# Kernel optimization log

Hardware: AMD Instinct MI355X
Metric: run time of the kernel (lower is better)

## Reference

```python
import jax, jax.numpy as jnp
import numpy as np

B, S, DIM = 2, 2048, 2048
QH, KVH = 32, 8
HD = DIM // QH            # 64
KV_DIM = HD * KVH         # 512
MAX_LEN = 2048
SCALE = HD ** -0.5
NEG_INF = -1e30


def _rope_cache(seq_len, head_dim, max_len, theta=10000.0, factor=8.0):
    # faithful to generate_sin_cos_pos_emb (causal branch, offset=0),
    # cache built at max_len then sliced to seq_len by the caller
    idx = np.arange(0, head_dim, 2, dtype=np.float64) / head_dim
    inv_freq = 1.0 / theta ** idx
    if factor > 1.0:
        seq_eff = max(max_len, max_len)  # generate called with seq_len=max_length
        adj = (factor * seq_eff / max_len - (factor - 1.0)) ** (head_dim / (head_dim - 2.0))
        inv_freq = 1.0 / (theta * adj) ** idx
    pos = np.arange(0, max_len, dtype=np.float64)
    freqs = np.einsum('i,j->ij', pos, inv_freq)
    emb = np.concatenate([freqs, freqs], axis=-1)  # [max_len, head_dim]
    cos = jnp.asarray(np.cos(emb)[:seq_len], dtype=jnp.float32)
    sin = jnp.asarray(np.sin(emb)[:seq_len], dtype=jnp.float32)
    return cos, sin


def _rotate_half(x):
    x1, x2 = jnp.split(x, 2, axis=-1)
    return jnp.concatenate([-x2, x1], axis=-1)


def _apply_rope(x, cos, sin):
    # x: [B, H, S, D]; cos/sin: [S, D]
    return x * cos + _rotate_half(x) * sin


def setup_inputs() -> dict:
    key = jax.random.key(0)
    ks = jax.random.split(key, 11)
    s = 0.02
    return {
        'query': jax.random.normal(ks[0], (B, S, DIM), jnp.float32),
        'key':   jax.random.normal(ks[1], (B, S, DIM), jnp.float32),
        'value': jax.random.normal(ks[2], (B, S, DIM), jnp.float32),
        'w_q': jax.random.normal(ks[3], (DIM, DIM), jnp.float32) * s,
        'b_q': jnp.zeros((DIM,), jnp.float32),
        'w_k': jax.random.normal(ks[4], (DIM, KV_DIM), jnp.float32) * s,
        'b_k': jnp.zeros((KV_DIM,), jnp.float32),
        'w_v': jax.random.normal(ks[5], (DIM, KV_DIM), jnp.float32) * s,
        'b_v': jnp.zeros((KV_DIM,), jnp.float32),
        'w_o': jax.random.normal(ks[6], (DIM, DIM), jnp.float32) * s,
        'b_o': jnp.zeros((DIM,), jnp.float32),
    }


def reference(query, key, value, w_q, b_q, w_k, b_k, w_v, b_v, w_o, b_o):
    # projections (weights stored as [in, out])
    q = query @ w_q + b_q                                    # [B,S,DIM]
    k = key   @ w_k + b_k                                    # [B,S,KV_DIM]
    v = value @ w_v + b_v                                    # [B,S,KV_DIM]

    q = q.reshape(B, S, QH, HD).transpose(0, 2, 1, 3)        # [B,QH,S,HD]
    k = k.reshape(B, S, KVH, HD).transpose(0, 2, 1, 3)       # [B,KVH,S,HD]
    v = v.reshape(B, S, KVH, HD).transpose(0, 2, 1, 3)       # [B,KVH,S,HD]

    cos, sin = _rope_cache(S, HD, MAX_LEN)
    q = _apply_rope(q, cos, sin)
    k = _apply_rope(k, cos, sin)

    # GQA: group queries per kv head (equivalent to repeat_interleave on K/V)
    G = QH // KVH
    qg = q.reshape(B, KVH, G, S, HD)
    scores = jnp.einsum('bhgqd,bhkd->bhgqk', qg, k) * SCALE  # [B,KVH,G,S,S]
    causal = jnp.tril(jnp.ones((S, S), dtype=bool))
    scores = jnp.where(causal, scores, NEG_INF)
    probs = jax.nn.softmax(scores, axis=-1)
    ctx = jnp.einsum('bhgqk,bhkd->bhgqd', probs, v)          # [B,KVH,G,S,HD]
    ctx = ctx.reshape(B, QH, S, HD).transpose(0, 2, 1, 3).reshape(B, S, DIM)
    return ctx @ w_o + b_o                                   # [B,S,DIM]
```

## Files before the change

kernel.cpp:

```cpp
#include <hip/hip_runtime.h>
#include <hip/hip_bf16.h>

typedef __hip_bfloat16 bf16_t;
typedef __attribute__((ext_vector_type(8))) short bf16x8;
typedef __attribute__((ext_vector_type(4))) float f32x4;

#define S_LEN   2048
#define D_MODEL 2048
#define N_QH    32
#define N_KVH   8
#define HEAD_D  64
#define KV_D    512
#define M_ROWS  4096
#define QK_SCALE (0.125f * 1.44269504088896340736f)
#define NQT     16

__global__ void rope_table_kernel(float* __restrict__ cosT, float* __restrict__ sinT) {
    int pos = blockIdx.x * 2 + (threadIdx.x >> 5);
    int j   = threadIdx.x & 31;
    double invf = pow(10000.0, -(double)(2 * j) / 64.0);
    double a = (double)pos * invf;
    cosT[pos * 32 + j] = (float)cos(a);
    sinT[pos * 32 + j] = (float)sin(a);
}

__global__ void wt_conv_all_kernel(const float* __restrict__ wq, const float* __restrict__ wk,
                                   const float* __restrict__ wv, const float* __restrict__ wo,
                                   bf16_t* __restrict__ tq, bf16_t* __restrict__ tk,
                                   bf16_t* __restrict__ tv, bf16_t* __restrict__ to) {
    __shared__ float tile[32][33];
    const int x = blockIdx.x;
    const float* W; bf16_t* Wt; int N, nb;
    if (x < 64)       { W = wq; Wt = tq; N = D_MODEL; nb = x; }
    else if (x < 80)  { W = wk; Wt = tk; N = KV_D;    nb = x - 64; }
    else if (x < 96)  { W = wv; Wt = tv; N = KV_D;    nb = x - 80; }
    else              { W = wo; Wt = to; N = D_MODEL; nb = x - 96; }
    const int K = D_MODEL;
    int n0 = nb * 32, k0 = blockIdx.y * 32;
    int tx = threadIdx.x & 31, ty = threadIdx.x >> 5;
#pragma unroll
    for (int i = 0; i < 4; i++) {
        int r = ty + i * 8;
        tile[r][tx] = W[(size_t)(k0 + r) * N + n0 + tx];
    }
    __syncthreads();
#pragma unroll
    for (int i = 0; i < 4; i++) {
        int r = ty + i * 8;
        Wt[(size_t)(n0 + r) * K + k0 + tx] = __float2bfloat16(tile[tx][r]);
    }
}

struct __align__(8) bf16x4s { bf16_t x, y, z, w; };

__device__ __forceinline__ void async_copy16(const bf16_t* g, bf16_t* l) {
    __builtin_amdgcn_global_load_lds((const __attribute__((address_space(1))) void*)g,
                                     (__attribute__((address_space(3))) void*)l, 16, 0, 0);
}

template <int ROPE, int OUTF32, int QSCALE>
__global__ __launch_bounds__(256, 2)
void gqa_gemm_kernel(const bf16_t* __restrict__ A, const bf16_t* __restrict__ Bt,
                     const float* __restrict__ bias, void* __restrict__ Cout,
                     int M, int N, int K,
                     const float* __restrict__ cosT, const float* __restrict__ sinT) {
    __shared__ __align__(16) bf16_t As[128 * 64];
    __shared__ __align__(16) bf16_t Bs[128 * 64];

    const int t = threadIdx.x;
    const int bx = blockIdx.x;
    const int xcd = bx & 7, j = bx >> 3;
    const int am0 = (((xcd >> 1) << 3) + (j >> 3)) * 128;
    const int bn0 = (((xcd & 1) << 3) + (j & 7)) * 128;

    const int l = t & 63, w = t >> 6;
    const int wr = w >> 1, wc = w & 1;
    const int lr = l & 15, lk = l >> 4;

    f32x4 acc[4][4];
#pragma unroll
    for (int i = 0; i < 4; i++)
#pragma unroll
        for (int jx = 0; jx < 4; jx++) acc[i][jx] = (f32x4)0.0f;

    const int r0 = t >> 3;
    const int c  = (t & 7) ^ (r0 & 7);
    const bf16_t* aptr = A + (size_t)(am0 + r0) * K + c * 8;
    const bf16_t* bptr = Bt + (size_t)(bn0 + r0) * K + c * 8;
    bf16_t* aLds = As + r0 * 64 + (t & 7) * 8;
    bf16_t* bLds = Bs + r0 * 64 + (t & 7) * 8;

    for (int k0 = 0; k0 < K; k0 += 64) {
#pragma unroll
        for (int s = 0; s < 4; ++s) {
            async_copy16(aptr + (size_t)(s * 32) * K + k0, aLds + s * 2048);
            async_copy16(bptr + (size_t)(s * 32) * K + k0, bLds + s * 2048);
        }
        __syncthreads();

        bf16x8 af[4][2], bfr[4][2];
#pragma unroll
        for (int mi = 0; mi < 4; mi++)
#pragma unroll
            for (int ks = 0; ks < 2; ks++)
                af[mi][ks] = *(const bf16x8*)&As[(wr * 64 + mi * 16 + lr) * 64 +
                                 ((ks * 32 + lk * 8) ^ ((lr & 7) << 3))];
#pragma unroll
        for (int ni = 0; ni < 4; ni++)
#pragma unroll
            for (int ks = 0; ks < 2; ks++)
                bfr[ni][ks] = *(const bf16x8*)&Bs[(wc * 64 + ni * 16 + lr) * 64 +
                                  ((ks * 32 + lk * 8) ^ ((lr & 7) << 3))];
#pragma unroll
        for (int mi = 0; mi < 4; mi++)
#pragma unroll
            for (int ni = 0; ni < 4; ni++)
#pragma unroll
                for (int ks = 0; ks < 2; ks++)
                    acc[mi][ni] = __builtin_amdgcn_mfma_f32_16x16x32_bf16(
                        af[mi][ks], bfr[ni][ks], acc[mi][ni], 0, 0, 0);
        __syncthreads();
    }

#pragma unroll
    for (int mi = 0; mi < 4; mi++) {
#pragma unroll
        for (int reg = 0; reg < 4; reg++) {
            int row = am0 + wr * 64 + mi * 16 + lk * 4 + reg;
            if (OUTF32) {
                float* out = (float*)Cout;
#pragma unroll
                for (int ni = 0; ni < 4; ni++) {
                    int col = bn0 + wc * 64 + ni * 16 + lr;
                    out[(size_t)row * N + col] = acc[mi][ni][reg] + bias[col];
                }
            } else if (ROPE) {
                bf16_t* out = (bf16_t*)Cout;
                int pos = row & (S_LEN - 1);
#pragma unroll
                for (int np = 0; np < 2; np++) {
                    int jj = np * 16 + lr;
                    float cs = cosT[pos * 32 + jj];
                    float sn = sinT[pos * 32 + jj];
                    int col1 = bn0 + wc * 64 + np * 16 + lr;
                    float x1 = acc[mi][np][reg] + bias[col1];
                    float x2 = acc[mi][np + 2][reg] + bias[col1 + 32];
                    float o1 = x1 * cs - x2 * sn;
                    float o2 = x2 * cs + x1 * sn;
                    if (QSCALE) { o1 *= QK_SCALE; o2 *= QK_SCALE; }
                    out[(size_t)row * N + col1]      = __float2bfloat16(o1);
                    out[(size_t)row * N + col1 + 32] = __float2bfloat16(o2);
                }
            } else {
                bf16_t* out = (bf16_t*)Cout;
#pragma unroll
                for (int ni = 0; ni < 4; ni++) {
                    int col = bn0 + wc * 64 + ni * 16 + lr;
                    out[(size_t)row * N + col] =
                        __float2bfloat16(acc[mi][ni][reg] + bias[col]);
                }
            }
        }
    }
}

__global__ __launch_bounds__(256, 2)
void gqa_kvc_kernel(const float* __restrict__ Key, const float* __restrict__ Val,
                    const float* __restrict__ Query,
                    const bf16_t* __restrict__ Wtk, const bf16_t* __restrict__ Wtv,
                    const float* __restrict__ bk, const float* __restrict__ bv,
                    bf16_t* __restrict__ Kout, bf16_t* __restrict__ VtOut,
                    bf16_t* __restrict__ Qbf,
                    const float* __restrict__ cosT, const float* __restrict__ sinT) {
    __shared__ __align__(16) char smem[33792];
    bf16_t* As = (bf16_t*)smem;
    bf16_t* Bs = (bf16_t*)(smem + 8192);
    float*  VtE = (float*)smem;

    const int bx = blockIdx.x;
    const int t = threadIdx.x;

    if (bx >= 512) {
        int tid = (bx - 512) * 256 + t;
        const int total = M_ROWS * D_MODEL / 4;
#pragma unroll 4
        for (int i = tid; i < total; i += 512 * 256) {
            float4 v = ((const float4*)Query)[i];
            bf16x4s o;
            o.x = __float2bfloat16(v.x);
            o.y = __float2bfloat16(v.y);
            o.z = __float2bfloat16(v.z);
            o.w = __float2bfloat16(v.w);
            ((bf16x4s*)Qbf)[i] = o;
        }
        return;
    }

    constexpr int K = D_MODEL;
    const int xcd = bx & 7;
    const int jj  = bx >> 3;
    const int z   = xcd >> 2;
    const int am0 = (((xcd & 3) << 3) + (jj >> 3)) * 128;
    const int bn0 = (jj & 7) * 64;

    const float* A32  = z ? Val : Key;
    const bf16_t* Bt  = z ? Wtv : Wtk;
    const float* bias = z ? bv : bk;

    const int l = t & 63, w = t >> 6;
    const int lr = l & 15, lk = l >> 4;

    f32x4 acc[2][4];
#pragma unroll
    for (int i = 0; i < 2; i++)
#pragma unroll
        for (int jx = 0; jx < 4; jx++) acc[i][jx] = (f32x4)0.0f;

    const int srow = t >> 2;
    const int scol = (t & 3) * 8;
    const float*  aptr = A32 + (size_t)(am0 + srow) * K + scol;
    const bf16_t* bptr = Bt + (size_t)(bn0 + srow) * K + scol;
    bf16_t* bLds = Bs + t * 8;

    for (int k0 = 0; k0 < K; k0 += 32) {
        async_copy16(bptr + k0, bLds);
#pragma unroll
        for (int rb = 0; rb < 2; ++rb) {
            const float* ap = aptr + (size_t)(rb * 64) * K + k0;
            float4 v0 = ((const float4*)ap)[0];
            float4 v1 = ((const float4*)ap)[1];
            union { bf16x8 v; bf16_t e[8]; } u;
            u.e[0] = __float2bfloat16(v0.x); u.e[1] = __float2bfloat16(v0.y);
            u.e[2] = __float2bfloat16(v0.z); u.e[3] = __float2bfloat16(v0.w);
            u.e[4] = __float2bfloat16(v1.x); u.e[5] = __float2bfloat16(v1.y);
            u.e[6] = __float2bfloat16(v1.z); u.e[7] = __float2bfloat16(v1.w);
            *(bf16x8*)&As[rb * 2048 + t * 8] = u.v;
        }
        __syncthreads();

        bf16x8 af[2], bfr[4];
#pragma unroll
        for (int mi = 0; mi < 2; mi++)
            af[mi] = *(const bf16x8*)&As[(w * 32 + mi * 16 + lr) * 32 + lk * 8];
#pragma unroll
        for (int ni = 0; ni < 4; ni++)
            bfr[ni] = *(const bf16x8*)&Bs[(ni * 16 + lr) * 32 + lk * 8];
#pragma unroll
        for (int mi = 0; mi < 2; mi++)
#pragma unroll
            for (int ni = 0; ni < 4; ni++)
                acc[mi][ni] = __builtin_amdgcn_mfma_f32_16x16x32_bf16(af[mi], bfr[ni],
                                                                      acc[mi][ni], 0, 0, 0);
        __syncthreads();
    }

    if (z == 0) {
#pragma unroll
        for (int mi = 0; mi < 2; mi++)
#pragma unroll
            for (int reg = 0; reg < 4; reg++) {
                int row = am0 + w * 32 + mi * 16 + lk * 4 + reg;
                int pos = row & (S_LEN - 1);
#pragma unroll
                for (int np = 0; np < 2; np++) {
                    int j = np * 16 + lr;
                    float cs = cosT[pos * 32 + j];
                    float sn = sinT[pos * 32 + j];
                    int col1 = bn0 + np * 16 + lr;
                    float x1 = acc[mi][np][reg] + bias[col1];
                    float x2 = acc[mi][np + 2][reg] + bias[col1 + 32];
                    Kout[(size_t)row * KV_D + col1]      = __float2bfloat16(x1 * cs - x2 * sn);
                    Kout[(size_t)row * KV_D + col1 + 32] = __float2bfloat16(x2 * cs + x1 * sn);
                }
            }
    } else {
#pragma unroll
        for (int mi = 0; mi < 2; mi++)
#pragma unroll
            for (int reg = 0; reg < 4; reg++)
#pragma unroll
                for (int ni = 0; ni < 4; ni++)
                    VtE[(w * 64 + ni * 16 + lr) * 33 + mi * 16 + lk * 4 + reg] =
                        acc[mi][ni][reg] + bias[bn0 + ni * 16 + lr];
        __syncthreads();
        const int d = l;
        const int bI = am0 >> 11;
        const int kvhI = bn0 >> 6;
        const int sl = (am0 & (S_LEN - 1)) + w * 32;
        bf16_t* dst = VtOut + ((size_t)(bI * N_KVH + kvhI) * HEAD_D + d) * S_LEN + sl;
        const float* src = &VtE[(w * 64 + d) * 33];
#pragma unroll
        for (int cc = 0; cc < 4; cc++) {
            union { bf16x8 v; bf16_t e[8]; } u;
#pragma unroll
            for (int j = 0; j < 8; j++) u.e[j] = __float2bfloat16(src[cc * 8 + j]);
            *(bf16x8*)(dst + cc * 8) = u.v;
        }
    }
}

__device__ __forceinline__ void stage_K8(const bf16_t* KB, bf16_t* dst, int kt, int t) {
    const int skey = t >> 3;
    const int c    = (t & 7) ^ (skey & 7);
    async_copy16(KB + (size_t)(kt * 64 + skey) * KV_D + c * 8, dst + t * 8);
}
__device__ __forceinline__ void stage_V8(const bf16_t* VTb, bf16_t* dst, int kt, int t) {
    const int sd = t >> 3;
    const int c  = (t & 7) ^ (sd & 7);
    async_copy16(VTb + (size_t)sd * S_LEN + kt * 64 + c * 8, dst + t * 8);
}

__global__ __launch_bounds__(512, 4)
void gqa_attn_kernel(const bf16_t* __restrict__ Q, const bf16_t* __restrict__ Kb,
                     const bf16_t* __restrict__ VT, bf16_t* __restrict__ Ctx) {
    __shared__ __align__(16) bf16_t Ks[2][64 * 64];
    __shared__ __align__(16) bf16_t Vs[2][64 * 64];
    __shared__ __align__(16) bf16_t Pw[8][16 * 72];

    const int t = threadIdx.x, l = t & 63, w = t >> 6;
    const int lr = l & 15, lk = l >> 4;

    const int flat = blockIdx.x;
    const int xcd = flat & 7, j0 = flat >> 3;
    const int combo  = xcd * 2 + (j0 >> 5);
    const int within = j0 & 31;
    const int b   = combo >> 3;
    const int kvh = combo & 7;
    const int h   = kvh * 4 + (within >> 3);
    const int p   = within & 7;

    const bf16_t* KB  = Kb + (size_t)b * S_LEN * KV_D + kvh * HEAD_D;
    const bf16_t* VTb = VT + ((size_t)(b * N_KVH + kvh) * HEAD_D) * S_LEN;

#pragma unroll
    for (int half = 0; half < 2; ++half) {
        const int qt  = half ? (NQT - 1 - p) : p;
        const int q0w = qt * 128 + w * 16;
        const int qg  = q0w + lr;

        bf16x8 qf[2];
        {
            const bf16_t* qrow = Q + ((size_t)(b * S_LEN + qg)) * D_MODEL + h * HEAD_D;
            qf[0] = *(const bf16x8*)(qrow + lk * 8);
            qf[1] = *(const bf16x8*)(qrow + 32 + lk * 8);
        }

        float lrow = 0.f;
        f32x4 oaccT[4];
#pragma unroll
        for (int df = 0; df < 4; df++) oaccT[df] = (f32x4)0.0f;

        const int nkt = 2 * qt + 2;

        stage_K8(KB, Ks[0], 0, t);
        stage_V8(VTb, Vs[0], 0, t);
        __syncthreads();

        int cur = 0;
        for (int kt = 0; kt < nkt; ++kt) {
            const bool pre = (kt + 1 < nkt);
            if (pre) {
                stage_K8(KB, Ks[cur ^ 1], kt + 1, t);
                stage_V8(VTb, Vs[cur ^ 1], kt + 1, t);
            }

            if (kt * 64 <= q0w + 15) {
                const bool diag = (kt * 64 + 63 > q0w);

                f32x4 sfrT[4];
#pragma unroll
                for (int ni = 0; ni < 4; ni++) sfrT[ni] = (f32x4)0.0f;
                __builtin_amdgcn_s_setprio(1);
#pragma unroll
                for (int ni = 0; ni < 4; ni++)
#pragma unroll
                    for (int ks = 0; ks < 2; ks++) {
                        bf16x8 kf = *(const bf16x8*)&Ks[cur][(ni * 16 + lr) * 64 +
                                        ((ks * 32 + lk * 8) ^ ((lr & 7) << 3))];
                        sfrT[ni] = __builtin_amdgcn_mfma_f32_16x16x32_bf16(kf, qf[ks],
                                                                           sfrT[ni], 0, 0, 0);
                    }
                __builtin_amdgcn_s_setprio(0);

                float rsp[4] = {0.f, 0.f, 0.f, 0.f};
                float pe[16];
#pragma unroll
                for (int ni = 0; ni < 4; ni++)
#pragma unroll
                    for (int r = 0; r < 4; r++) {
                        float sc = sfrT[ni][r];
                        if (diag) {
                            int keyg = kt * 64 + ni * 16 + lk * 4 + r;
                            if (keyg > qg) sc = -1e30f;
                        }
                        float e = exp2f(sc);
                        pe[ni * 4 + r] = e;
                        rsp[ni] += e;
                    }
                float rs = (rsp[0] + rsp[1]) + (rsp[2] + rsp[3]);
                rs += __shfl_xor(rs, 16);
                rs += __shfl_xor(rs, 32);
                lrow += rs;

#pragma unroll
                for (int ni = 0; ni < 4; ni++) {
                    bf16x4s pk;
                    pk.x = __float2bfloat16(pe[ni * 4 + 0]);
                    pk.y = __float2bfloat16(pe[ni * 4 + 1]);
                    pk.z = __float2bfloat16(pe[ni * 4 + 2]);
                    pk.w = __float2bfloat16(pe[ni * 4 + 3]);
                    *(bf16x4s*)&Pw[w][lr * 72 + ni * 16 + lk * 4] = pk;
                }

                __builtin_amdgcn_s_setprio(1);
#pragma unroll
                for (int ks = 0; ks < 2; ks++) {
                    bf16x8 pf = *(const bf16x8*)&Pw[w][lr * 72 + ks * 32 + lk * 8];
#pragma unroll
                    for (int df = 0; df < 4; df++) {
                        bf16x8 vf = *(const bf16x8*)&Vs[cur][(df * 16 + lr) * 64 +
                                        ((ks * 32 + lk * 8) ^ ((lr & 7) << 3))];
                        oaccT[df] = __builtin_amdgcn_mfma_f32_16x16x32_bf16(vf, pf,
                                            oaccT[df], 0, 0, 0);
                    }
                }
                __builtin_amdgcn_s_setprio(0);
            }

            __syncthreads();
            cur ^= 1;
        }

        {
            float inv = 1.0f / lrow;
            bf16_t* crow = Ctx + ((size_t)(b * S_LEN + qg)) * D_MODEL + h * HEAD_D;
#pragma unroll
            for (int df = 0; df < 4; df++) {
                bf16x4s ov;
                ov.x = __float2bfloat16(oaccT[df][0] * inv);
                ov.y = __float2bfloat16(oaccT[df][1] * inv);
                ov.z = __float2bfloat16(oaccT[df][2] * inv);
                ov.w = __float2bfloat16(oaccT[df][3] * inv);
                *(bf16x4s*)(crow + df * 16 + lk * 4) = ov;
            }
        }
    }
}

extern "C" void kernel_launch(void* const* d_in, const int* in_sizes, int n_in,
                              void* d_out, int out_size, void* d_ws, size_t ws_size,
                              hipStream_t stream) {
    const float* query = (const float*)d_in[0];
    const float* key_  = (const float*)d_in[1];
    const float* value = (const float*)d_in[2];
    const float* w_q = (const float*)d_in[3];
    const float* b_q = (const float*)d_in[4];
    const float* w_k = (const float*)d_in[5];
    const float* b_k = (const float*)d_in[6];
    const float* w_v = (const float*)d_in[7];
    const float* b_v = (const float*)d_in[8];
    const float* w_o = (const float*)d_in[9];
    const float* b_o = (const float*)d_in[10];
    float* out = (float*)d_out;

    char* ws = (char*)d_ws;
    bf16_t* Abuf = (bf16_t*)(ws);
    bf16_t* qb   = (bf16_t*)(ws + (size_t)(16 << 20));
    bf16_t* kb   = (bf16_t*)(ws + (size_t)(32 << 20));
    bf16_t* vt   = (bf16_t*)(ws + (size_t)(36 << 20));
    bf16_t* wtq  = (bf16_t*)(ws + (size_t)(40 << 20));
    bf16_t* wtk  = (bf16_t*)(ws + (size_t)(48 << 20));
    bf16_t* wtv  = (bf16_t*)(ws + (size_t)(50 << 20));
    bf16_t* wto  = (bf16_t*)(ws + (size_t)(52 << 20));
    float* cosT  = (float*)(ws + (size_t)(60 << 20));
    float* sinT  = (float*)(ws + (size_t)(60 << 20) + (256 << 10));

    rope_table_kernel<<<S_LEN / 2, 64, 0, stream>>>(cosT, sinT);

    wt_conv_all_kernel<<<dim3(160, 64), 256, 0, stream>>>(w_q, w_k, w_v, w_o,
                                                          wtq, wtk, wtv, wto);

    gqa_kvc_kernel<<<1024, 256, 0, stream>>>(key_, value, query, wtk, wtv,
                                             b_k, b_v, kb, vt, Abuf, cosT, sinT);

    gqa_gemm_kernel<1, 0, 1><<<512, 256, 0, stream>>>(
        Abuf, wtq, b_q, qb, M_ROWS, D_MODEL, D_MODEL, cosT, sinT);

    gqa_attn_kernel<<<512, 512, 0, stream>>>(qb, kb, vt, Abuf);

    gqa_gemm_kernel<0, 1, 0><<<512, 256, 0, stream>>>(
        Abuf, wto, b_o, out, M_ROWS, D_MODEL, D_MODEL, cosT, sinT);
}
```

Before: 226.0 us.

## Shrink K/V projection tiles to 64x64 and prefetch fp32 A tile in registers

The K/V projection kernel moves from 128x64 to 64x64 output tiles, doubling the GEMM block count and cutting LDS use so that four blocks can share a CU. The next fp32 A slice is now loaded into registers during the current iteration, with explicit waitcnt and barriers to overlap that load with the MFMAs. The V transpose staging now goes through a bf16 LDS buffer rather than fp32. Smaller tiles mean each block reuses less of the fp32 inputs and weights, so global traffic goes up in exchange for more parallelism and latency hiding.

New measurement: 215.5 us. -4.7%, faster.

```diff
diff --git a/kernel.cpp b/kernel.cpp
--- a/kernel.cpp
+++ b/kernel.cpp
@@ -164,7 +164,7 @@
     }
 }
 
-__global__ __launch_bounds__(256, 2)
+__global__ __launch_bounds__(256, 4)
 void gqa_kvc_kernel(const float* __restrict__ Key, const float* __restrict__ Val,
                     const float* __restrict__ Query,
                     const bf16_t* __restrict__ Wtk, const bf16_t* __restrict__ Wtv,
@@ -172,16 +172,16 @@
                     bf16_t* __restrict__ Kout, bf16_t* __restrict__ VtOut,
                     bf16_t* __restrict__ Qbf,
                     const float* __restrict__ cosT, const float* __restrict__ sinT) {
-    __shared__ __align__(16) char smem[33792];
-    bf16_t* As = (bf16_t*)smem;
-    bf16_t* Bs = (bf16_t*)(smem + 8192);
-    float*  VtE = (float*)smem;
+    __shared__ __align__(16) char smem[9216];
+    bf16_t* As  = (bf16_t*)smem;
+    bf16_t* Bs  = (bf16_t*)(smem + 4096);
+    bf16_t* VtE = (bf16_t*)smem;
 
     const int bx = blockIdx.x;
     const int t = threadIdx.x;
 
-    if (bx >= 512) {
-        int tid = (bx - 512) * 256 + t;
+    if (bx >= 1024) {
+        int tid = (bx - 1024) * 256 + t;
         const int total = M_ROWS * D_MODEL / 4;
 #pragma unroll 4
         for (int i = tid; i < total; i += 512 * 256) {
@@ -198,10 +198,10 @@
 
     constexpr int K = D_MODEL;
     const int xcd = bx & 7;
-    const int jj  = bx >> 3;
+    const int j   = bx >> 3;
     const int z   = xcd >> 2;
-    const int am0 = (((xcd & 3) << 3) + (jj >> 3)) * 128;
-    const int bn0 = (jj & 7) * 64;
+    const int am0 = (((xcd & 3) << 4) + (j >> 3)) * 64;
+    const int bn0 = (j & 7) * 64;
 
     const float* A32  = z ? Val : Key;
     const bf16_t* Bt  = z ? Wtv : Wtk;
@@ -210,92 +210,92 @@
     const int l = t & 63, w = t >> 6;
     const int lr = l & 15, lk = l >> 4;
 
-    f32x4 acc[2][4];
-#pragma unroll
-    for (int i = 0; i < 2; i++)
-#pragma unroll
-        for (int jx = 0; jx < 4; jx++) acc[i][jx] = (f32x4)0.0f;
-
-    const int srow = t >> 2;
-    const int scol = (t & 3) * 8;
-    const float*  aptr = A32 + (size_t)(am0 + srow) * K + scol;
-    const bf16_t* bptr = Bt + (size_t)(bn0 + srow) * K + scol;
+    f32x4 acc[4];
+#pragma unroll
+    for (int jx = 0; jx < 4; jx++) acc[jx] = (f32x4)0.0f;
+
+    const int sr = t >> 2;
+    const int sc = (t & 3) * 8;
+    const float*  aptr = A32 + (size_t)(am0 + sr) * K + sc;
+    const bf16_t* bptr = Bt + (size_t)(bn0 + sr) * K + sc;
+    bf16_t* aLds = As + sr * 32 + sc;
     bf16_t* bLds = Bs + t * 8;
 
-    for (int k0 = 0; k0 < K; k0 += 32) {
-        async_copy16(bptr + k0, bLds);
-#pragma unroll
-        for (int rb = 0; rb < 2; ++rb) {
-            const float* ap = aptr + (size_t)(rb * 64) * K + k0;
-            float4 v0 = ((const float4*)ap)[0];
-            float4 v1 = ((const float4*)ap)[1];
-            union { bf16x8 v; bf16_t e[8]; } u;
-            u.e[0] = __float2bfloat16(v0.x); u.e[1] = __float2bfloat16(v0.y);
-            u.e[2] = __float2bfloat16(v0.z); u.e[3] = __float2bfloat16(v0.w);
-            u.e[4] = __float2bfloat16(v1.x); u.e[5] = __float2bfloat16(v1.y);
-            u.e[6] = __float2bfloat16(v1.z); u.e[7] = __float2bfloat16(v1.w);
-            *(bf16x8*)&As[rb * 2048 + t * 8] = u.v;
-        }
-        __syncthreads();
-
-        bf16x8 af[2], bfr[4];
-#pragma unroll
-        for (int mi = 0; mi < 2; mi++)
-            af[mi] = *(const bf16x8*)&As[(w * 32 + mi * 16 + lr) * 32 + lk * 8];
+    float4 pa0 = ((const float4*)aptr)[0];
+    float4 pa1 = ((const float4*)aptr)[1];
+
+    for (int it = 0; it < K / 32; ++it) {
+        union { bf16x8 v; bf16_t e[8]; } u;
+        u.e[0] = __float2bfloat16(pa0.x); u.e[1] = __float2bfloat16(pa0.y);
+        u.e[2] = __float2bfloat16(pa0.z); u.e[3] = __float2bfloat16(pa0.w);
+        u.e[4] = __float2bfloat16(pa1.x); u.e[5] = __float2bfloat16(pa1.y);
+        u.e[6] = __float2bfloat16(pa1.z); u.e[7] = __float2bfloat16(pa1.w);
+        *(bf16x8*)aLds = u.v;
+        async_copy16(bptr + it * 32, bLds);
+        __builtin_amdgcn_sched_barrier(0);
+        if (it + 1 < K / 32) {
+            const float* ap = aptr + (it + 1) * 32;
+            pa0 = ((const float4*)ap)[0];
+            pa1 = ((const float4*)ap)[1];
+            __builtin_amdgcn_sched_barrier(0);
+            asm volatile("s_waitcnt lgkmcnt(0) vmcnt(2)" ::: "memory");
+        } else {
+            asm volatile("s_waitcnt lgkmcnt(0) vmcnt(0)" ::: "memory");
+        }
+        __builtin_amdgcn_sched_barrier(0);
+        __builtin_amdgcn_s_barrier();
+        __builtin_amdgcn_sched_barrier(0);
+
+        bf16x8 af = *(const bf16x8*)&As[(w * 16 + lr) * 32 + lk * 8];
+        bf16x8 bfr[4];
 #pragma unroll
         for (int ni = 0; ni < 4; ni++)
             bfr[ni] = *(const bf16x8*)&Bs[(ni * 16 + lr) * 32 + lk * 8];
 #pragma unroll
-        for (int mi = 0; mi < 2; mi++)
-#pragma unroll
-            for (int ni = 0; ni < 4; ni++)
-                acc[mi][ni] = __builtin_amdgcn_mfma_f32_16x16x32_bf16(af[mi], bfr[ni],
-                                                                      acc[mi][ni], 0, 0, 0);
+        for (int ni = 0; ni < 4; ni++)
+            acc[ni] = __builtin_amdgcn_mfma_f32_16x16x32_bf16(af, bfr[ni], acc[ni], 0, 0, 0);
+        __builtin_amdgcn_sched_barrier(0);
+        __builtin_amdgcn_s_barrier();
+        __builtin_amdgcn_sched_barrier(0);
+    }
+
+    if (z == 0) {
+#pragma unroll
+        for (int reg = 0; reg < 4; reg++) {
+            int row = am0 + w * 16 + lk * 4 + reg;
+            int pos = row & (S_LEN - 1);
+#pragma unroll
+            for (int np = 0; np < 2; np++) {
+                int jj = np * 16 + lr;
+                float cs = cosT[pos * 32 + jj];
+                float sn = sinT[pos * 32 + jj];
+                int col1 = bn0 + np * 16 + lr;
+                float x1 = acc[np][reg] + bias[col1];
+                float x2 = acc[np + 2][reg] + bias[col1 + 32];
+                Kout[(size_t)row * KV_D + col1]      = __float2bfloat16(x1 * cs - x2 * sn);
+                Kout[(size_t)row * KV_D + col1 + 32] = __float2bfloat16(x2 * cs + x1 * sn);
+            }
+        }
+    } else {
         __syncthreads();
-    }
-
-    if (z == 0) {
-#pragma unroll
-        for (int mi = 0; mi < 2; mi++)
-#pragma unroll
-            for (int reg = 0; reg < 4; reg++) {
-                int row = am0 + w * 32 + mi * 16 + lk * 4 + reg;
-                int pos = row & (S_LEN - 1);
-#pragma unroll
-                for (int np = 0; np < 2; np++) {
-                    int j = np * 16 + lr;
-                    float cs = cosT[pos * 32 + j];
-                    float sn = sinT[pos * 32 + j];
-                    int col1 = bn0 + np * 16 + lr;
-                    float x1 = acc[mi][np][reg] + bias[col1];
-                    float x2 = acc[mi][np + 2][reg] + bias[col1 + 32];
-                    Kout[(size_t)row * KV_D + col1]      = __float2bfloat16(x1 * cs - x2 * sn);
-                    Kout[(size_t)row * KV_D + col1 + 32] = __float2bfloat16(x2 * cs + x1 * sn);
-                }
-            }
-    } else {
-#pragma unroll
-        for (int mi = 0; mi < 2; mi++)
-#pragma unroll
-            for (int reg = 0; reg < 4; reg++)
-#pragma unroll
-                for (int ni = 0; ni < 4; ni++)
-                    VtE[(w * 64 + ni * 16 + lr) * 33 + mi * 16 + lk * 4 + reg] =
-                        acc[mi][ni][reg] + bias[bn0 + ni * 16 + lr];
+#pragma unroll
+        for (int ni = 0; ni < 4; ni++) {
+            bf16x4s pk;
+            pk.x = __float2bfloat16(acc[ni][0] + bias[bn0 + ni * 16 + lr]);
+            pk.y = __float2bfloat16(acc[ni][1] + bias[bn0 + ni * 16 + lr]);
+            pk.z = __float2bfloat16(acc[ni][2] + bias[bn0 + ni * 16 + lr]);
+            pk.w = __float2bfloat16(acc[ni][3] + bias[bn0 + ni * 16 + lr]);
+            *(bf16x4s*)&VtE[(ni * 16 + lr) * 72 + w * 16 + lk * 4] = pk;
+        }
         __syncthreads();
-        const int d = l;
+        const int d = t & 63, w2 = t >> 6;
         const int bI = am0 >> 11;
         const int kvhI = bn0 >> 6;
-        const int sl = (am0 & (S_LEN - 1)) + w * 32;
+        const int sl = (am0 & (S_LEN - 1)) + w2 * 16;
         bf16_t* dst = VtOut + ((size_t)(bI * N_KVH + kvhI) * HEAD_D + d) * S_LEN + sl;
-        const float* src = &VtE[(w * 64 + d) * 33];
-#pragma unroll
-        for (int cc = 0; cc < 4; cc++) {
-            union { bf16x8 v; bf16_t e[8]; } u;
-#pragma unroll
-            for (int j = 0; j < 8; j++) u.e[j] = __float2bfloat16(src[cc * 8 + j]);
-            *(bf16x8*)(dst + cc * 8) = u.v;
-        }
+        const bf16_t* src = &VtE[d * 72 + w2 * 16];
+        *(bf16x8*)dst       = *(const bf16x8*)src;
+        *(bf16x8*)(dst + 8) = *(const bf16x8*)(src + 8);
     }
 }
 
@@ -480,7 +480,7 @@
     wt_conv_all_kernel<<<dim3(160, 64), 256, 0, stream>>>(w_q, w_k, w_v, w_o,
                                                           wtq, wtk, wtv, wto);
 
-    gqa_kvc_kernel<<<1024, 256, 0, stream>>>(key_, value, query, wtk, wtv,
+    gqa_kvc_kernel<<<1536, 256, 0, stream>>>(key_, value, query, wtk, wtv,
                                              b_k, b_v, kb, vt, Abuf, cosT, sinT);
 
     gqa_gemm_kernel<1, 0, 1><<<512, 256, 0, stream>>>(
```
